# Performance work log

Measured on AMD Instinct MI355X. Metric: run time of the kernel, lower is better.

Reference implementation:

```python
import jax, jax.numpy as jnp
import numpy as np
from jax import lax

NC1, NC2, NC3 = 64, 64, 512
TEMP = 1.0
EPS = 1e-5
B = 256


def setup_inputs() -> dict:
    key = jax.random.key(0)
    ks = jax.random.split(key, 16)
    d = {}
    d["inp"] = jax.random.normal(ks[0], (B, 3, 32, 32), jnp.float32)
    d["conv1_w"] = jax.random.normal(ks[1], (6, 3, 5, 5), jnp.float32) * 0.1
    d["conv1_b"] = jax.random.normal(ks[2], (6,), jnp.float32) * 0.1
    d["bn1_g"] = jnp.ones((6,), jnp.float32)
    d["bn1_b"] = jnp.zeros((6,), jnp.float32)
    d["conv2_w"] = jax.random.normal(ks[3], (16, 6, 5, 5), jnp.float32) * 0.1
    d["conv2_b"] = jax.random.normal(ks[4], (16,), jnp.float32) * 0.1
    d["bn2_g"] = jnp.ones((16,), jnp.float32)
    d["bn2_b"] = jnp.zeros((16,), jnp.float32)
    d["fc1_w"] = jax.random.normal(ks[5], (120, 400), jnp.float32) * 0.05
    d["fc1_b"] = jax.random.normal(ks[6], (120,), jnp.float32) * 0.05
    d["fc2_w"] = jax.random.normal(ks[7], (10, 120), jnp.float32) * 0.05
    d["fc2_b"] = jax.random.normal(ks[8], (10,), jnp.float32) * 0.05
    d["k1s"] = jax.random.normal(ks[9], (NC1, 6), jnp.float32)
    d["k2s"] = jax.random.normal(ks[10], (NC2, 16), jnp.float32)
    d["k3s"] = jax.random.normal(ks[11], (NC3, 120), jnp.float32)
    return d


def _conv(x, w, b):
    y = lax.conv_general_dilated(x, w, (1, 1), 'VALID',
                                 dimension_numbers=('NCHW', 'OIHW', 'NCHW'))
    return y + b[None, :, None, None]


def _bn_train(x, g, b):
    # BatchNorm2d in training mode: biased batch stats over (N,H,W)
    mean = x.mean(axis=(0, 2, 3), keepdims=True)
    var = ((x - mean) ** 2).mean(axis=(0, 2, 3), keepdims=True)
    return (x - mean) / jnp.sqrt(var + EPS) * g[None, :, None, None] + b[None, :, None, None]


def _maxpool2(x):
    return lax.reduce_window(x, -jnp.inf, lax.max, (1, 1, 2, 2), (1, 1, 2, 2), 'VALID')


def _codebook_logits_spatial(act, keys):
    # act: [B,C,H,W], keys: [K,C] -> -||act - k||_2 over C -> [B,K,H,W]
    diff = act[:, None] - keys[None, :, :, None, None]
    return -jnp.sqrt((diff ** 2).sum(axis=2))


def _neural_gas_loss(v, temp):
    n_clusters = v.shape[1]
    weightings = jnp.exp(-jnp.arange(n_clusters, dtype=v.dtype) / temp)
    sorted_v = jnp.sort(v, axis=1)
    return (sorted_v ** 2 * weightings).sum(axis=1)


def reference(inp, conv1_w, conv1_b, bn1_g, bn1_b, conv2_w, conv2_b, bn2_g, bn2_b,
              fc1_w, fc1_b, fc2_w, fc2_b, k1s, k2s, k3s):
    act1 = _bn_train(_conv(inp, conv1_w, conv1_b), bn1_g, bn1_b)          # [B,6,28,28]
    act_logits1 = _codebook_logits_spatial(act1, k1s)                     # [B,NC1,28,28]
    x = _maxpool2(jax.nn.relu(act1))                                      # [B,6,14,14]
    act2 = _bn_train(_conv(x, conv2_w, conv2_b), bn2_g, bn2_b)            # [B,16,10,10]
    act_logits2 = _codebook_logits_spatial(act2, k2s)                     # [B,NC2,10,10]
    x = _maxpool2(jax.nn.relu(act2))                                      # [B,16,5,5]
    x = x.reshape(x.shape[0], -1)                                         # [B,400]
    act3 = x @ fc1_w.T + fc1_b                                            # [B,120]
    diff3 = act3[:, None, :] - k3s[None, :, :]
    act_logits3 = -jnp.sqrt((diff3 ** 2).sum(axis=2))                     # [B,NC3]
    x = jax.nn.relu(act3)
    act4 = x @ fc2_w.T + fc2_b                                            # [B,10]
    # ARGS.ng branch: neural-gas cluster loss + argmax assignments
    cluster_loss = _neural_gas_loss(act_logits3, TEMP)                    # [B]
    assignments = jnp.argmax(act_logits3, axis=1)                         # [B] int
    return (assignments, cluster_loss.mean(), act4, act_logits1, act_logits2, act_logits3)
```

## Files before the change

kernel.cpp:

```cpp
#include <hip/hip_runtime.h>

#define B 256
#define EPSV 1e-5f

#define OFF_ASSIGN 0
#define OFF_LOSS   256
#define OFF_ACT4   257
#define OFF_L1     2817
#define OFF_L2     12847873
#define OFF_L3     14486273

__device__ inline void wave_reduce2(float& s, float& q) {
#pragma unroll
    for (int o = 32; o > 0; o >>= 1) {
        s += __shfl_down(s, o, 64);
        q += __shfl_down(q, o, 64);
    }
}

__global__ __launch_bounds__(256) void conv1_kernel(
        const float* __restrict__ inp, const float* __restrict__ w,
        const float* __restrict__ bias, float* __restrict__ c1,
        float* __restrict__ part,
        const float* __restrict__ w1, const float* __restrict__ k3,
        float* __restrict__ w1t, float* __restrict__ k3st) {
    int bc = blockIdx.x;
    int tid = threadIdx.x;
    if (bc >= 1536) {
        int idx = (bc - 1536) * 256 + tid;
        if (idx < 48000) {
            int c = idx / 120, o = idx % 120;
            w1t[idx] = w1[o * 400 + c];
        } else if (idx < 48000 + 61440) {
            int j = idx - 48000;
            int c = j >> 9, k = j & 511;
            k3st[j] = k3[k * 120 + c];
        }
        return;
    }
    int b = bc / 6, c = bc % 6;
    __shared__ float ws[75];
    __shared__ float rs[4], rq[4];
    if (tid < 75) ws[tid] = w[c * 75 + tid];
    __syncthreads();
    const float* ip = inp + b * 3072;
    float bs = bias[c];
    float s = 0.f, sq = 0.f;
    for (int hw = tid; hw < 784; hw += 256) {
        int oh = hw / 28, ow = hw % 28;
        float acc = bs;
#pragma unroll
        for (int ic = 0; ic < 3; ++ic) {
            const float* ipc = ip + ic * 1024 + oh * 32 + ow;
            const float* wc = ws + ic * 25;
#pragma unroll
            for (int kh = 0; kh < 5; ++kh)
#pragma unroll
                for (int kw = 0; kw < 5; ++kw)
                    acc += ipc[kh * 32 + kw] * wc[kh * 5 + kw];
        }
        c1[bc * 784 + hw] = acc;
        s += acc; sq += acc * acc;
    }
    wave_reduce2(s, sq);
    if ((tid & 63) == 0) { rs[tid >> 6] = s; rq[tid >> 6] = sq; }
    __syncthreads();
    if (tid == 0) {
        part[bc * 2]     = rs[0] + rs[1] + rs[2] + rs[3];
        part[bc * 2 + 1] = rq[0] + rq[1] + rq[2] + rq[3];
    }
}

__global__ __launch_bounds__(1024) void stage1_kernel(
        const float* __restrict__ c1raw, const float* __restrict__ part1,
        const float* __restrict__ g1, const float* __restrict__ bb1,
        const float* __restrict__ k1s,
        const float* __restrict__ c2w, const float* __restrict__ c2b,
        float* __restrict__ outL1, float* __restrict__ c2,
        float* __restrict__ part2) {
    int b = blockIdx.x, tid = threadIdx.x;
    int lane = tid & 63, wid = tid >> 6;
    __shared__ float act[4704];
    __shared__ float sk[384];
    __shared__ float w2s[2400];
    __shared__ float xp[1176];
    __shared__ float sa[1600];
    __shared__ float chs[6], chq[6], ssc[6], ssh[6];
    if (wid < 6) {
        float s = 0.f, q = 0.f;
#pragma unroll
        for (int j = 0; j < 4; ++j) {
            int bi = lane + 64 * j;
            s += part1[(bi * 6 + wid) * 2];
            q += part1[(bi * 6 + wid) * 2 + 1];
        }
        wave_reduce2(s, q);
        if (lane == 0) { chs[wid] = s; chq[wid] = q; }
    }
    for (int i = tid; i < 384; i += 1024) sk[i] = k1s[i];
    for (int i = tid; i < 2400; i += 1024) w2s[i] = c2w[i];
    __syncthreads();
    if (tid < 6) {
        float m = chs[tid] * (1.f / 200704.f);
        float v = chq[tid] * (1.f / 200704.f) - m * m;
        float sc = g1[tid] * rsqrtf(v + EPSV);
        ssc[tid] = sc; ssh[tid] = bb1[tid] - m * sc;
    }
    __syncthreads();
    const float* cp = c1raw + b * 4704;
    for (int i = tid; i < 4704; i += 1024) {
        int c = i / 784;
        act[i] = cp[i] * ssc[c] + ssh[c];
    }
    __syncthreads();
    float* op = outL1 + (long)b * 50176;
    for (int i = tid; i < 50176; i += 1024) {
        int k = i / 784, hw = i - k * 784;
        const float* kp = sk + k * 6;
        float d0 = act[hw] - kp[0];
        float d1 = act[784 + hw] - kp[1];
        float d2 = act[1568 + hw] - kp[2];
        float d3 = act[2352 + hw] - kp[3];
        float d4 = act[3136 + hw] - kp[4];
        float d5 = act[3920 + hw] - kp[5];
        float s = d0 * d0 + d1 * d1 + d2 * d2 + d3 * d3 + d4 * d4 + d5 * d5;
        op[i] = -sqrtf(s);
    }
    for (int i = tid; i < 1176; i += 1024) {
        int c = i / 196, p = i % 196, ph = p / 14, pw = p % 14;
        const float* ap = act + c * 784 + ph * 56 + pw * 2;
        float m = fmaxf(fmaxf(ap[0], ap[1]), fmaxf(ap[28], ap[29]));
        xp[i] = fmaxf(m, 0.f);
    }
    __syncthreads();
    for (int i = tid; i < 1600; i += 1024) {
        int c = i / 100, hw = i - c * 100;
        int oh = hw / 10, ow = hw - oh * 10;
        float acc = c2b[c];
#pragma unroll
        for (int ic = 0; ic < 6; ++ic) {
            const float* xsrc = xp + ic * 196 + oh * 14 + ow;
            const float* wp = w2s + c * 150 + ic * 25;
#pragma unroll
            for (int kh = 0; kh < 5; ++kh)
#pragma unroll
                for (int kw = 0; kw < 5; ++kw)
                    acc += xsrc[kh * 14 + kw] * wp[kh * 5 + kw];
        }
        sa[i] = acc;
    }
    __syncthreads();
    for (int i = tid; i < 1600; i += 1024) c2[b * 1600 + i] = sa[i];
    {
        float s = 0.f, q = 0.f;
        if (lane < 100) { float x = sa[wid * 100 + lane]; s = x; q = x * x; }
        if (lane < 36)  { float x = sa[wid * 100 + 64 + lane]; s += x; q += x * x; }
        wave_reduce2(s, q);
        if (lane == 0) {
            part2[(b * 16 + wid) * 2]     = s;
            part2[(b * 16 + wid) * 2 + 1] = q;
        }
    }
}

__global__ __launch_bounds__(1024) void stage2_kernel(
        const float* __restrict__ c2, const float* __restrict__ part2,
        const float* __restrict__ g2, const float* __restrict__ bb2,
        const float* __restrict__ k2s,
        const float* __restrict__ w1t, const float* __restrict__ f1b,
        const float* __restrict__ f2w, const float* __restrict__ f2b,
        const float* __restrict__ k3st,
        float* __restrict__ outL2, float* __restrict__ outAct4,
        float* __restrict__ outL3, float* __restrict__ outAssign,
        float* __restrict__ lossb) {
    int b = blockIdx.x, tid = threadIdx.x;
    int lane = tid & 63, wid = tid >> 6;
    __shared__ float sa[1600];
    __shared__ float sk[1024];
    __shared__ float xs[400];
    __shared__ float chs[16], chq[16], ssc[16], ssh[16];
    __shared__ float partq[8][128];
    __shared__ float a3r[120], a3p[120];
    __shared__ float pv[2][512];
    __shared__ float sv[512];
    __shared__ int   cntp[2][512];
    __shared__ float wsum[8], wmv[8];
    __shared__ int wmi[8];
    {
        float s = 0.f, q = 0.f;
#pragma unroll
        for (int j = 0; j < 4; ++j) {
            int bi = lane + 64 * j;
            s += part2[(bi * 16 + wid) * 2];
            q += part2[(bi * 16 + wid) * 2 + 1];
        }
        wave_reduce2(s, q);
        if (lane == 0) { chs[wid] = s; chq[wid] = q; }
    }
    for (int i = tid; i < 1024; i += 1024) sk[i] = k2s[i];
    __syncthreads();
    if (tid < 16) {
        float m = chs[tid] * (1.f / 25600.f);
        float v = chq[tid] * (1.f / 25600.f) - m * m;
        float sc = g2[tid] * rsqrtf(v + EPSV);
        ssc[tid] = sc; ssh[tid] = bb2[tid] - m * sc;
    }
    __syncthreads();
    for (int i = tid; i < 1600; i += 1024) {
        int c = i / 100;
        sa[i] = c2[b * 1600 + i] * ssc[c] + ssh[c];
    }
    __syncthreads();
    float* op2 = outL2 + (long)b * 6400;
    for (int i = tid; i < 6400; i += 1024) {
        int k = i / 100, hw = i - k * 100;
        float s = 0.f;
#pragma unroll
        for (int c = 0; c < 16; ++c) {
            float d = sa[c * 100 + hw] - sk[k * 16 + c];
            s += d * d;
        }
        op2[i] = -sqrtf(s);
    }
    for (int i = tid; i < 400; i += 1024) {
        int c = i / 25, p = i % 25, ph = p / 5, pw = p % 5;
        const float* ap = sa + c * 100 + ph * 20 + pw * 2;
        float m = fmaxf(fmaxf(ap[0], ap[1]), fmaxf(ap[10], ap[11]));
        xs[i] = fmaxf(m, 0.f);
    }
    __syncthreads();
    {
        int o = tid & 127, q8 = tid >> 7;
        float s = 0.f;
        if (o < 120) {
            const float* wp = w1t + (q8 * 50) * 120 + o;
            const float* xp2 = xs + q8 * 50;
#pragma unroll 10
            for (int c = 0; c < 50; ++c) s += xp2[c] * wp[c * 120];
        }
        partq[q8][o] = s;
    }
    __syncthreads();
    if (tid < 120) {
        float acc = f1b[tid];
#pragma unroll
        for (int q8 = 0; q8 < 8; ++q8) acc += partq[q8][tid];
        a3r[tid] = acc;
        a3p[tid] = fmaxf(acc, 0.f);
    }
    __syncthreads();
    {
        int k = tid & 511, h = tid >> 9;
        const float* kp = k3st + k;
        float s = 0.f;
#pragma unroll 10
        for (int c = 0; c < 60; ++c) {
            int cc = h * 60 + c;
            float d = a3r[cc] - kp[cc * 512];
            s += d * d;
        }
        pv[h][k] = s;
    }
    if (tid < 10) {
        float acc = f2b[tid];
        const float* wp = f2w + tid * 120;
#pragma unroll 8
        for (int c = 0; c < 120; ++c) acc += a3p[c] * wp[c];
        outAct4[b * 10 + tid] = acc;
    }
    __syncthreads();
    if (tid < 512) {
        float v = -sqrtf(pv[0][tid] + pv[1][tid]);
        sv[tid] = v;
        outL3[(long)b * 512 + tid] = v;
    }
    __syncthreads();
    {
        int i = tid & 511, h = tid >> 9;
        float v = sv[i];
        const float4* sv4 = reinterpret_cast<const float4*>(sv);
        int cnt = 0;
#pragma unroll 8
        for (int j4 = h * 64; j4 < h * 64 + 64; ++j4) {
            float4 o4 = sv4[j4];
            int jb = j4 * 4;
            cnt += (o4.x < v || (o4.x == v && jb < i)) ? 1 : 0;
            cnt += (o4.y < v || (o4.y == v && jb + 1 < i)) ? 1 : 0;
            cnt += (o4.z < v || (o4.z == v && jb + 2 < i)) ? 1 : 0;
            cnt += (o4.w < v || (o4.w == v && jb + 3 < i)) ? 1 : 0;
        }
        cntp[h][i] = cnt;
    }
    __syncthreads();
    if (tid < 512) {
        float v = sv[tid];
        int cnt = cntp[0][tid] + cntp[1][tid];
        float contrib = v * v * expf(-(float)cnt);
        float ssum = contrib;
#pragma unroll
        for (int o = 32; o > 0; o >>= 1) ssum += __shfl_down(ssum, o, 64);
        float mv = v; int mi = tid;
#pragma unroll
        for (int o = 32; o > 0; o >>= 1) {
            float ov = __shfl_down(mv, o, 64);
            int oi = __shfl_down(mi, o, 64);
            if (ov > mv || (ov == mv && oi < mi)) { mv = ov; mi = oi; }
        }
        if (lane == 0) { wsum[wid] = ssum; wmv[wid] = mv; wmi[wid] = mi; }
    }
    __syncthreads();
    if (tid == 0) {
        float tot = 0.f;
        float bmv = wmv[0]; int bmi = wmi[0];
#pragma unroll
        for (int w = 0; w < 8; ++w) {
            tot += wsum[w];
            if (wmv[w] > bmv || (wmv[w] == bmv && wmi[w] < bmi)) { bmv = wmv[w]; bmi = wmi[w]; }
        }
        lossb[b] = tot;
        outAssign[b] = (float)bmi;
    }
}

__global__ void final_kernel(const float* __restrict__ loss_b, float* __restrict__ out_loss) {
    __shared__ float r[256];
    int tid = threadIdx.x;
    r[tid] = loss_b[tid];
    __syncthreads();
    for (int s = 128; s > 0; s >>= 1) {
        if (tid < s) r[tid] += r[tid + s];
        __syncthreads();
    }
    if (tid == 0) out_loss[0] = r[0] / 256.f;
}

extern "C" void kernel_launch(void* const* d_in, const int* in_sizes, int n_in,
                              void* d_out, int out_size, void* d_ws, size_t ws_size,
                              hipStream_t stream) {
    const float* inp = (const float*)d_in[0];
    const float* c1w = (const float*)d_in[1];
    const float* c1b = (const float*)d_in[2];
    const float* g1  = (const float*)d_in[3];
    const float* bb1 = (const float*)d_in[4];
    const float* c2w = (const float*)d_in[5];
    const float* c2b = (const float*)d_in[6];
    const float* g2  = (const float*)d_in[7];
    const float* bb2 = (const float*)d_in[8];
    const float* f1w = (const float*)d_in[9];
    const float* f1b = (const float*)d_in[10];
    const float* f2w = (const float*)d_in[11];
    const float* f2b = (const float*)d_in[12];
    const float* k1  = (const float*)d_in[13];
    const float* k2  = (const float*)d_in[14];
    const float* k3  = (const float*)d_in[15];
    float* out = (float*)d_out;

    float* W = (float*)d_ws;
    float* c1raw = W;
    float* part1 = c1raw + 1204224;
    float* c2raw = part1 + 3072;
    float* part2 = c2raw + 409600;
    float* lossb = part2 + 8192;
    float* w1t   = lossb + 256;
    float* k3st  = w1t + 48000;

    conv1_kernel<<<1964, 256, 0, stream>>>(inp, c1w, c1b, c1raw, part1,
                                           f1w, k3, w1t, k3st);
    stage1_kernel<<<B, 1024, 0, stream>>>(c1raw, part1, g1, bb1, k1, c2w, c2b,
                                          out + OFF_L1, c2raw, part2);
    stage2_kernel<<<B, 1024, 0, stream>>>(c2raw, part2, g2, bb2, k2,
                                          w1t, f1b, f2w, f2b, k3st,
                                          out + OFF_L2, out + OFF_ACT4,
                                          out + OFF_L3, out + OFF_ASSIGN, lossb);
    final_kernel<<<1, 256, 0, stream>>>(lossb, out + OFF_LOSS);
}
```

Before: 94.49 us.

## Fuse all stages into one persistent kernel with software grid barriers

Replaces the four kernel launches with a single 256-block kernel that keeps each sample's conv1 and conv2 activations in shared memory. Device-wide atomic barriers stand in for the launch boundaries needed by the batch-norm statistics, and the final loss reduction is done by block 0 after an atomic counter wait. This removes launch gaps and the global round trips of the conv1 and conv2 intermediates. In exchange, all 256 blocks must be co-resident for the spin barriers to be safe, block size drops from 1024 to 512, and a memset is added to reset the barrier counters.

```diff
diff --git a/kernel.cpp b/kernel.cpp
--- a/kernel.cpp
+++ b/kernel.cpp
@@ -10,7 +10,7 @@
 #define OFF_L2     12847873
 #define OFF_L3     14486273
 
-__device__ inline void wave_reduce2(float& s, float& q) {
+__device__ __forceinline__ void wave_reduce2(float& s, float& q) {
 #pragma unroll
     for (int o = 32; o > 0; o >>= 1) {
         s += __shfl_down(s, o, 64);
@@ -18,74 +18,110 @@
     }
 }
 
-__global__ __launch_bounds__(256) void conv1_kernel(
-        const float* __restrict__ inp, const float* __restrict__ w,
-        const float* __restrict__ bias, float* __restrict__ c1,
-        float* __restrict__ part,
-        const float* __restrict__ w1, const float* __restrict__ k3,
-        float* __restrict__ w1t, float* __restrict__ k3st) {
-    int bc = blockIdx.x;
-    int tid = threadIdx.x;
-    if (bc >= 1536) {
-        int idx = (bc - 1536) * 256 + tid;
-        if (idx < 48000) {
-            int c = idx / 120, o = idx % 120;
-            w1t[idx] = w1[o * 400 + c];
-        } else if (idx < 48000 + 61440) {
-            int j = idx - 48000;
-            int c = j >> 9, k = j & 511;
-            k3st[j] = k3[k * 120 + c];
-        }
-        return;
-    }
-    int b = bc / 6, c = bc % 6;
-    __shared__ float ws[75];
-    __shared__ float rs[4], rq[4];
-    if (tid < 75) ws[tid] = w[c * 75 + tid];
-    __syncthreads();
-    const float* ip = inp + b * 3072;
-    float bs = bias[c];
-    float s = 0.f, sq = 0.f;
-    for (int hw = tid; hw < 784; hw += 256) {
-        int oh = hw / 28, ow = hw % 28;
-        float acc = bs;
-#pragma unroll
-        for (int ic = 0; ic < 3; ++ic) {
-            const float* ipc = ip + ic * 1024 + oh * 32 + ow;
-            const float* wc = ws + ic * 25;
-#pragma unroll
-            for (int kh = 0; kh < 5; ++kh)
-#pragma unroll
-                for (int kw = 0; kw < 5; ++kw)
-                    acc += ipc[kh * 32 + kw] * wc[kh * 5 + kw];
-        }
-        c1[bc * 784 + hw] = acc;
-        s += acc; sq += acc * acc;
-    }
-    wave_reduce2(s, sq);
-    if ((tid & 63) == 0) { rs[tid >> 6] = s; rq[tid >> 6] = sq; }
-    __syncthreads();
-    if (tid == 0) {
-        part[bc * 2]     = rs[0] + rs[1] + rs[2] + rs[3];
-        part[bc * 2 + 1] = rq[0] + rq[1] + rq[2] + rq[3];
-    }
+__device__ __forceinline__ void gbar(unsigned* cnt, unsigned* gen) {
+    __syncthreads();
+    if (threadIdx.x == 0) {
+        __threadfence();
+        unsigned g = __hip_atomic_load(gen, __ATOMIC_RELAXED, __HIP_MEMORY_SCOPE_AGENT);
+        unsigned a = __hip_atomic_fetch_add(cnt, 1u, __ATOMIC_ACQ_REL, __HIP_MEMORY_SCOPE_AGENT);
+        if (a == gridDim.x - 1) {
+            __hip_atomic_store(cnt, 0u, __ATOMIC_RELAXED, __HIP_MEMORY_SCOPE_AGENT);
+            __hip_atomic_fetch_add(gen, 1u, __ATOMIC_RELEASE, __HIP_MEMORY_SCOPE_AGENT);
+        } else {
+            while (__hip_atomic_load(gen, __ATOMIC_ACQUIRE, __HIP_MEMORY_SCOPE_AGENT) == g)
+                __builtin_amdgcn_s_sleep(1);
+        }
+    }
+    __syncthreads();
 }
 
-__global__ __launch_bounds__(1024) void stage1_kernel(
-        const float* __restrict__ c1raw, const float* __restrict__ part1,
-        const float* __restrict__ g1, const float* __restrict__ bb1,
-        const float* __restrict__ k1s,
-        const float* __restrict__ c2w, const float* __restrict__ c2b,
-        float* __restrict__ outL1, float* __restrict__ c2,
-        float* __restrict__ part2) {
+__global__ __launch_bounds__(512, 4) void fused_kernel(
+        const float* __restrict__ inp, const float* __restrict__ c1w,
+        const float* __restrict__ c1b, const float* __restrict__ g1,
+        const float* __restrict__ bb1, const float* __restrict__ c2w,
+        const float* __restrict__ c2b, const float* __restrict__ g2,
+        const float* __restrict__ bb2, const float* __restrict__ f1w,
+        const float* __restrict__ f1b, const float* __restrict__ f2w,
+        const float* __restrict__ f2b, const float* __restrict__ k1s,
+        const float* __restrict__ k2s, const float* __restrict__ k3s,
+        float* __restrict__ out, unsigned* __restrict__ bar,
+        float* __restrict__ part1, float* __restrict__ part2,
+        float* __restrict__ lossb, float* __restrict__ w1t,
+        float* __restrict__ k3st) {
     int b = blockIdx.x, tid = threadIdx.x;
     int lane = tid & 63, wid = tid >> 6;
-    __shared__ float act[4704];
-    __shared__ float sk[384];
+
+    __shared__ __align__(16) float si[3072];
+    __shared__ __align__(16) float act[4704];
+    __shared__ float cw[450];
+    __shared__ float cb1[6];
+    __shared__ float sk1[384];
     __shared__ float w2s[2400];
+    __shared__ float c2bs[16];
     __shared__ float xp[1176];
     __shared__ float sa[1600];
-    __shared__ float chs[6], chq[6], ssc[6], ssh[6];
+    __shared__ float wpart[96];
+    __shared__ float chs[16], chq[16], ssc[16], ssh[16];
+    __shared__ float a3r[120], a3p[120];
+    __shared__ float wsum[8], wmv[8];
+    __shared__ int wmi[8];
+    __shared__ float rfin[256];
+    float* sk2   = si;
+    float* xs    = si + 1024;
+    float* partq = si + 1424;
+    float* sv    = si + 1936;
+
+    for (int i = tid; i < 3072; i += 512) si[i] = inp[b * 3072 + i];
+    for (int i = tid; i < 450; i += 512) cw[i] = c1w[i];
+    if (tid < 6) cb1[tid] = c1b[tid];
+    if (tid < 16) c2bs[tid] = c2b[tid];
+    for (int i = tid; i < 384; i += 512) sk1[i] = k1s[i];
+    for (int i = tid; i < 2400; i += 512) w2s[i] = c2w[i];
+    {
+        int idx = b * 428 + tid;
+        if (tid < 428 && idx < 109440) {
+            if (idx < 48000) { int c = idx / 120, o = idx % 120; w1t[idx] = f1w[o * 400 + c]; }
+            else { int j = idx - 48000; int c = j >> 9, k = j & 511; k3st[j] = k3s[k * 120 + c]; }
+        }
+    }
+    __syncthreads();
+    float s6[6], q6[6];
+#pragma unroll
+    for (int c = 0; c < 6; ++c) { s6[c] = 0.f; q6[c] = 0.f; }
+#pragma unroll
+    for (int c = 0; c < 6; ++c) {
+        for (int hw = tid; hw < 784; hw += 512) {
+            int oh = hw / 28, ow = hw % 28;
+            float acc = cb1[c];
+#pragma unroll
+            for (int ic = 0; ic < 3; ++ic) {
+                const float* ip = si + ic * 1024 + oh * 32 + ow;
+                const float* wp = cw + c * 75 + ic * 25;
+#pragma unroll
+                for (int kh = 0; kh < 5; ++kh)
+#pragma unroll
+                    for (int kw = 0; kw < 5; ++kw)
+                        acc += ip[kh * 32 + kw] * wp[kh * 5 + kw];
+            }
+            act[c * 784 + hw] = acc;
+            s6[c] += acc; q6[c] += acc * acc;
+        }
+    }
+#pragma unroll
+    for (int c = 0; c < 6; ++c) {
+        wave_reduce2(s6[c], q6[c]);
+        if (lane == 0) { wpart[(wid * 6 + c) * 2] = s6[c]; wpart[(wid * 6 + c) * 2 + 1] = q6[c]; }
+    }
+    __syncthreads();
+    if (tid < 6) {
+        float S = 0.f, Q = 0.f;
+#pragma unroll
+        for (int w = 0; w < 8; ++w) { S += wpart[(w * 6 + tid) * 2]; Q += wpart[(w * 6 + tid) * 2 + 1]; }
+        part1[(b * 6 + tid) * 2] = S;
+        part1[(b * 6 + tid) * 2 + 1] = Q;
+    }
+    gbar(bar + 0, bar + 1);
+
     if (wid < 6) {
         float s = 0.f, q = 0.f;
 #pragma unroll
@@ -97,8 +133,6 @@
         wave_reduce2(s, q);
         if (lane == 0) { chs[wid] = s; chq[wid] = q; }
     }
-    for (int i = tid; i < 384; i += 1024) sk[i] = k1s[i];
-    for (int i = tid; i < 2400; i += 1024) w2s[i] = c2w[i];
     __syncthreads();
     if (tid < 6) {
         float m = chs[tid] * (1.f / 200704.f);
@@ -107,36 +141,34 @@
         ssc[tid] = sc; ssh[tid] = bb1[tid] - m * sc;
     }
     __syncthreads();
-    const float* cp = c1raw + b * 4704;
-    for (int i = tid; i < 4704; i += 1024) {
+    for (int i = tid; i < 4704; i += 512) {
         int c = i / 784;
-        act[i] = cp[i] * ssc[c] + ssh[c];
-    }
-    __syncthreads();
-    float* op = outL1 + (long)b * 50176;
-    for (int i = tid; i < 50176; i += 1024) {
+        act[i] = act[i] * ssc[c] + ssh[c];
+    }
+    __syncthreads();
+    float* op = out + OFF_L1 + (long)b * 50176;
+    for (int i = tid; i < 50176; i += 512) {
         int k = i / 784, hw = i - k * 784;
-        const float* kp = sk + k * 6;
-        float d0 = act[hw] - kp[0];
-        float d1 = act[784 + hw] - kp[1];
+        const float* kp = sk1 + k * 6;
+        float d0 = act[hw]        - kp[0];
+        float d1 = act[784 + hw]  - kp[1];
         float d2 = act[1568 + hw] - kp[2];
         float d3 = act[2352 + hw] - kp[3];
         float d4 = act[3136 + hw] - kp[4];
         float d5 = act[3920 + hw] - kp[5];
-        float s = d0 * d0 + d1 * d1 + d2 * d2 + d3 * d3 + d4 * d4 + d5 * d5;
-        op[i] = -sqrtf(s);
-    }
-    for (int i = tid; i < 1176; i += 1024) {
+        op[i] = -sqrtf(d0*d0 + d1*d1 + d2*d2 + d3*d3 + d4*d4 + d5*d5);
+    }
+    for (int i = tid; i < 1176; i += 512) {
         int c = i / 196, p = i % 196, ph = p / 14, pw = p % 14;
         const float* ap = act + c * 784 + ph * 56 + pw * 2;
         float m = fmaxf(fmaxf(ap[0], ap[1]), fmaxf(ap[28], ap[29]));
         xp[i] = fmaxf(m, 0.f);
     }
     __syncthreads();
-    for (int i = tid; i < 1600; i += 1024) {
+    for (int i = tid; i < 1600; i += 512) {
         int c = i / 100, hw = i - c * 100;
         int oh = hw / 10, ow = hw - oh * 10;
-        float acc = c2b[c];
+        float acc = c2bs[c];
 #pragma unroll
         for (int ic = 0; ic < 6; ++ic) {
             const float* xsrc = xp + ic * 196 + oh * 14 + ow;
@@ -150,54 +182,31 @@
         sa[i] = acc;
     }
     __syncthreads();
-    for (int i = tid; i < 1600; i += 1024) c2[b * 1600 + i] = sa[i];
-    {
+#pragma unroll
+    for (int r = 0; r < 2; ++r) {
+        int cc = wid * 2 + r;
         float s = 0.f, q = 0.f;
-        if (lane < 100) { float x = sa[wid * 100 + lane]; s = x; q = x * x; }
-        if (lane < 36)  { float x = sa[wid * 100 + 64 + lane]; s += x; q += x * x; }
+        if (lane < 100) { float x = sa[cc * 100 + lane]; s = x; q = x * x; }
+        if (lane < 36)  { float x = sa[cc * 100 + 64 + lane]; s += x; q += x * x; }
         wave_reduce2(s, q);
-        if (lane == 0) {
-            part2[(b * 16 + wid) * 2]     = s;
-            part2[(b * 16 + wid) * 2 + 1] = q;
-        }
-    }
-}
-
-__global__ __launch_bounds__(1024) void stage2_kernel(
-        const float* __restrict__ c2, const float* __restrict__ part2,
-        const float* __restrict__ g2, const float* __restrict__ bb2,
-        const float* __restrict__ k2s,
-        const float* __restrict__ w1t, const float* __restrict__ f1b,
-        const float* __restrict__ f2w, const float* __restrict__ f2b,
-        const float* __restrict__ k3st,
-        float* __restrict__ outL2, float* __restrict__ outAct4,
-        float* __restrict__ outL3, float* __restrict__ outAssign,
-        float* __restrict__ lossb) {
-    int b = blockIdx.x, tid = threadIdx.x;
-    int lane = tid & 63, wid = tid >> 6;
-    __shared__ float sa[1600];
-    __shared__ float sk[1024];
-    __shared__ float xs[400];
-    __shared__ float chs[16], chq[16], ssc[16], ssh[16];
-    __shared__ float partq[8][128];
-    __shared__ float a3r[120], a3p[120];
-    __shared__ float pv[2][512];
-    __shared__ float sv[512];
-    __shared__ int   cntp[2][512];
-    __shared__ float wsum[8], wmv[8];
-    __shared__ int wmi[8];
-    {
+        if (lane == 0) { part2[(b * 16 + cc) * 2] = s; part2[(b * 16 + cc) * 2 + 1] = q; }
+    }
+    gbar(bar + 2, bar + 3);
+
+#pragma unroll
+    for (int r = 0; r < 2; ++r) {
+        int ch = wid + r * 8;
         float s = 0.f, q = 0.f;
 #pragma unroll
         for (int j = 0; j < 4; ++j) {
             int bi = lane + 64 * j;
-            s += part2[(bi * 16 + wid) * 2];
-            q += part2[(bi * 16 + wid) * 2 + 1];
+            s += part2[(bi * 16 + ch) * 2];
+            q += part2[(bi * 16 + ch) * 2 + 1];
         }
         wave_reduce2(s, q);
-        if (lane == 0) { chs[wid] = s; chq[wid] = q; }
-    }
-    for (int i = tid; i < 1024; i += 1024) sk[i] = k2s[i];
+        if (lane == 0) { chs[ch] = s; chq[ch] = q; }
+    }
+    for (int i = tid; i < 1024; i += 512) sk2[i] = k2s[i];
     __syncthreads();
     if (tid < 16) {
         float m = chs[tid] * (1.f / 25600.f);
@@ -206,23 +215,20 @@
         ssc[tid] = sc; ssh[tid] = bb2[tid] - m * sc;
     }
     __syncthreads();
-    for (int i = tid; i < 1600; i += 1024) {
+    for (int i = tid; i < 1600; i += 512) {
         int c = i / 100;
-        sa[i] = c2[b * 1600 + i] * ssc[c] + ssh[c];
-    }
-    __syncthreads();
-    float* op2 = outL2 + (long)b * 6400;
-    for (int i = tid; i < 6400; i += 1024) {
+        sa[i] = sa[i] * ssc[c] + ssh[c];
+    }
+    __syncthreads();
+    float* op2 = out + OFF_L2 + (long)b * 6400;
+    for (int i = tid; i < 6400; i += 512) {
         int k = i / 100, hw = i - k * 100;
         float s = 0.f;
 #pragma unroll
-        for (int c = 0; c < 16; ++c) {
-            float d = sa[c * 100 + hw] - sk[k * 16 + c];
-            s += d * d;
-        }
+        for (int c = 0; c < 16; ++c) { float d = sa[c * 100 + hw] - sk2[k * 16 + c]; s += d * d; }
         op2[i] = -sqrtf(s);
     }
-    for (int i = tid; i < 400; i += 1024) {
+    for (int i = tid; i < 400; i += 512) {
         int c = i / 25, p = i % 25, ph = p / 5, pw = p % 5;
         const float* ap = sa + c * 100 + ph * 20 + pw * 2;
         float m = fmaxf(fmaxf(ap[0], ap[1]), fmaxf(ap[10], ap[11]));
@@ -230,84 +236,64 @@
     }
     __syncthreads();
     {
-        int o = tid & 127, q8 = tid >> 7;
+        int o = tid & 127, q4 = tid >> 7;
         float s = 0.f;
         if (o < 120) {
-            const float* wp = w1t + (q8 * 50) * 120 + o;
-            const float* xp2 = xs + q8 * 50;
+            const float* wp = w1t + (q4 * 100) * 120 + o;
+            const float* xq = xs + q4 * 100;
 #pragma unroll 10
-            for (int c = 0; c < 50; ++c) s += xp2[c] * wp[c * 120];
-        }
-        partq[q8][o] = s;
+            for (int c = 0; c < 100; ++c) s += xq[c] * wp[c * 120];
+        }
+        partq[q4 * 128 + o] = s;
     }
     __syncthreads();
     if (tid < 120) {
-        float acc = f1b[tid];
-#pragma unroll
-        for (int q8 = 0; q8 < 8; ++q8) acc += partq[q8][tid];
+        float acc = f1b[tid] + partq[tid] + partq[128 + tid] + partq[256 + tid] + partq[384 + tid];
         a3r[tid] = acc;
         a3p[tid] = fmaxf(acc, 0.f);
     }
     __syncthreads();
+    float v;
     {
-        int k = tid & 511, h = tid >> 9;
-        const float* kp = k3st + k;
+        const float* kp = k3st + tid;
         float s = 0.f;
-#pragma unroll 10
-        for (int c = 0; c < 60; ++c) {
-            int cc = h * 60 + c;
-            float d = a3r[cc] - kp[cc * 512];
-            s += d * d;
-        }
-        pv[h][k] = s;
+#pragma unroll 8
+        for (int c = 0; c < 120; ++c) { float d = a3r[c] - kp[c * 512]; s += d * d; }
+        v = -sqrtf(s);
+        sv[tid] = v;
+        out[OFF_L3 + (long)b * 512 + tid] = v;
     }
     if (tid < 10) {
         float acc = f2b[tid];
         const float* wp = f2w + tid * 120;
 #pragma unroll 8
         for (int c = 0; c < 120; ++c) acc += a3p[c] * wp[c];
-        outAct4[b * 10 + tid] = acc;
-    }
-    __syncthreads();
-    if (tid < 512) {
-        float v = -sqrtf(pv[0][tid] + pv[1][tid]);
-        sv[tid] = v;
-        outL3[(long)b * 512 + tid] = v;
-    }
-    __syncthreads();
-    {
-        int i = tid & 511, h = tid >> 9;
-        float v = sv[i];
-        const float4* sv4 = reinterpret_cast<const float4*>(sv);
-        int cnt = 0;
+        out[OFF_ACT4 + b * 10 + tid] = acc;
+    }
+    __syncthreads();
+    const float4* sv4 = reinterpret_cast<const float4*>(sv);
+    int cnt = 0;
 #pragma unroll 8
-        for (int j4 = h * 64; j4 < h * 64 + 64; ++j4) {
-            float4 o4 = sv4[j4];
-            int jb = j4 * 4;
-            cnt += (o4.x < v || (o4.x == v && jb < i)) ? 1 : 0;
-            cnt += (o4.y < v || (o4.y == v && jb + 1 < i)) ? 1 : 0;
-            cnt += (o4.z < v || (o4.z == v && jb + 2 < i)) ? 1 : 0;
-            cnt += (o4.w < v || (o4.w == v && jb + 3 < i)) ? 1 : 0;
-        }
-        cntp[h][i] = cnt;
-    }
-    __syncthreads();
-    if (tid < 512) {
-        float v = sv[tid];
-        int cnt = cntp[0][tid] + cntp[1][tid];
-        float contrib = v * v * expf(-(float)cnt);
-        float ssum = contrib;
-#pragma unroll
-        for (int o = 32; o > 0; o >>= 1) ssum += __shfl_down(ssum, o, 64);
-        float mv = v; int mi = tid;
-#pragma unroll
-        for (int o = 32; o > 0; o >>= 1) {
-            float ov = __shfl_down(mv, o, 64);
-            int oi = __shfl_down(mi, o, 64);
-            if (ov > mv || (ov == mv && oi < mi)) { mv = ov; mi = oi; }
-        }
-        if (lane == 0) { wsum[wid] = ssum; wmv[wid] = mv; wmi[wid] = mi; }
-    }
+    for (int j4 = 0; j4 < 128; ++j4) {
+        float4 o4 = sv4[j4];
+        int jb = j4 * 4;
+        cnt += (o4.x < v || (o4.x == v && jb < tid)) ? 1 : 0;
+        cnt += (o4.y < v || (o4.y == v && jb + 1 < tid)) ? 1 : 0;
+        cnt += (o4.z < v || (o4.z == v && jb + 2 < tid)) ? 1 : 0;
+        cnt += (o4.w < v || (o4.w == v && jb + 3 < tid)) ? 1 : 0;
+    }
+    float contrib = v * v * expf(-(float)cnt);
+    float ssum = contrib;
+#pragma unroll
+    for (int o = 32; o > 0; o >>= 1) ssum += __shfl_down(ssum, o, 64);
+    float mv = v; int mi = tid;
+#pragma unroll
+    for (int o = 32; o > 0; o >>= 1) {
+        float ov = __shfl_down(mv, o, 64);
+        int oi = __shfl_down(mi, o, 64);
+        if (ov > mv || (ov == mv && oi < mi)) { mv = ov; mi = oi; }
+    }
+    if (lane == 0) { wsum[wid] = ssum; wmv[wid] = mv; wmi[wid] = mi; }
     __syncthreads();
     if (tid == 0) {
         float tot = 0.f;
@@ -318,20 +304,27 @@
             if (wmv[w] > bmv || (wmv[w] == bmv && wmi[w] < bmi)) { bmv = wmv[w]; bmi = wmi[w]; }
         }
         lossb[b] = tot;
-        outAssign[b] = (float)bmi;
-    }
-}
-
-__global__ void final_kernel(const float* __restrict__ loss_b, float* __restrict__ out_loss) {
-    __shared__ float r[256];
-    int tid = threadIdx.x;
-    r[tid] = loss_b[tid];
-    __syncthreads();
-    for (int s = 128; s > 0; s >>= 1) {
-        if (tid < s) r[tid] += r[tid + s];
+        out[OFF_ASSIGN + b] = (float)bmi;
+    }
+    __syncthreads();
+
+    if (tid == 0) {
+        __threadfence();
+        __hip_atomic_fetch_add(bar + 4, 1u, __ATOMIC_ACQ_REL, __HIP_MEMORY_SCOPE_AGENT);
+    }
+    if (b != 0) return;
+    if (tid == 0) {
+        while (__hip_atomic_load(bar + 4, __ATOMIC_ACQUIRE, __HIP_MEMORY_SCOPE_AGENT) < 256u)
+            __builtin_amdgcn_s_sleep(1);
+    }
+    __syncthreads();
+    if (tid < 256) rfin[tid] = lossb[tid];
+    __syncthreads();
+    for (int s2 = 128; s2 > 0; s2 >>= 1) {
+        if (tid < s2 && tid < 256) rfin[tid] += rfin[tid + s2];
         __syncthreads();
     }
-    if (tid == 0) out_loss[0] = r[0] / 256.f;
+    if (tid == 0) out[OFF_LOSS] = rfin[0] * (1.f / 256.f);
 }
 
 extern "C" void kernel_launch(void* const* d_in, const int* in_sizes, int n_in,
@@ -356,21 +349,15 @@
     float* out = (float*)d_out;
 
     float* W = (float*)d_ws;
-    float* c1raw = W;
-    float* part1 = c1raw + 1204224;
-    float* c2raw = part1 + 3072;
-    float* part2 = c2raw + 409600;
-    float* lossb = part2 + 8192;
-    float* w1t   = lossb + 256;
-    float* k3st  = w1t + 48000;
-
-    conv1_kernel<<<1964, 256, 0, stream>>>(inp, c1w, c1b, c1raw, part1,
-                                           f1w, k3, w1t, k3st);
-    stage1_kernel<<<B, 1024, 0, stream>>>(c1raw, part1, g1, bb1, k1, c2w, c2b,
-                                          out + OFF_L1, c2raw, part2);
-    stage2_kernel<<<B, 1024, 0, stream>>>(c2raw, part2, g2, bb2, k2,
-                                          w1t, f1b, f2w, f2b, k3st,
-                                          out + OFF_L2, out + OFF_ACT4,
-                                          out + OFF_L3, out + OFF_ASSIGN, lossb);
-    final_kernel<<<1, 256, 0, stream>>>(lossb, out + OFF_LOSS);
+    unsigned* bar = (unsigned*)d_ws;
+    float* part1 = W + 64;
+    float* part2 = W + 3136;
+    float* lossb = W + 11328;
+    float* w1t   = W + 11584;
+    float* k3st  = W + 59584;
+
+    hipMemsetAsync(d_ws, 0, 64, stream);
+    fused_kernel<<<B, 512, 0, stream>>>(inp, c1w, c1b, g1, bb1, c2w, c2b, g2, bb2,
+                                        f1w, f1b, f2w, f2b, k1, k2, k3,
+                                        out, bar, part1, part2, lossb, w1t, k3st);
 }
```

After: 151.3 us. 1.6x slower.

## Split per-sample stage kernels across more blocks and use dot-product distance expansion

Applied to the files above, without the earlier changes.

Stage1 now launches four 512-thread blocks per sample, and each block writes a quarter of the 64 codebook-1 distance maps. Only the first block of each sample goes on to compute conv2. Stage2 uses three blocks per sample: two compute halves of the codebook-2 distances and one handles the FC layers, codebook-3 and the ranking. Distances are computed as ||a||^2 + ||k||^2 - 2·a·k, which cuts per-element work but adds cancellation risk, clamped at zero. The split also spreads work across more CUs, at the cost of re-normalizing the activations redundantly in every block.

```diff
diff --git a/kernel.cpp b/kernel.cpp
--- a/kernel.cpp
+++ b/kernel.cpp
@@ -10,7 +10,7 @@
 #define OFF_L2     12847873
 #define OFF_L3     14486273
 
-__device__ inline void wave_reduce2(float& s, float& q) {
+__device__ __forceinline__ void wave_reduce2(float& s, float& q) {
 #pragma unroll
     for (int o = 32; o > 0; o >>= 1) {
         s += __shfl_down(s, o, 64);
@@ -71,21 +71,24 @@
     }
 }
 
-__global__ __launch_bounds__(1024) void stage1_kernel(
+__global__ __launch_bounds__(512) void stage1_kernel(
         const float* __restrict__ c1raw, const float* __restrict__ part1,
         const float* __restrict__ g1, const float* __restrict__ bb1,
         const float* __restrict__ k1s,
         const float* __restrict__ c2w, const float* __restrict__ c2b,
-        float* __restrict__ outL1, float* __restrict__ c2,
+        float* __restrict__ out, float* __restrict__ c2raw,
         float* __restrict__ part2) {
-    int b = blockIdx.x, tid = threadIdx.x;
+    int b = blockIdx.x >> 2, h = blockIdx.x & 3;
+    int tid = threadIdx.x;
     int lane = tid & 63, wid = tid >> 6;
-    __shared__ float act[4704];
-    __shared__ float sk[384];
+    __shared__ __align__(16) float act[4704];
+    __shared__ float sk1[384], k2sq1[64];
+    __shared__ float chs[6], chq[6], ssc[6], ssh[6];
+    __shared__ float xp[1176];
     __shared__ float w2s[2400];
-    __shared__ float xp[1176];
-    __shared__ float sa[1600];
-    __shared__ float chs[6], chq[6], ssc[6], ssh[6];
+    if (tid < 384) sk1[tid] = k1s[tid];
+    if (h == 0) for (int i = tid; i < 2400; i += 512) w2s[i] = c2w[i];
+    __syncthreads();
     if (wid < 6) {
         float s = 0.f, q = 0.f;
 #pragma unroll
@@ -97,8 +100,13 @@
         wave_reduce2(s, q);
         if (lane == 0) { chs[wid] = s; chq[wid] = q; }
     }
-    for (int i = tid; i < 384; i += 1024) sk[i] = k1s[i];
-    for (int i = tid; i < 2400; i += 1024) w2s[i] = c2w[i];
+    if (tid >= 384 && tid < 448) {
+        int k = tid - 384;
+        float s = 0.f;
+#pragma unroll
+        for (int c = 0; c < 6; ++c) { float x = sk1[k * 6 + c]; s += x * x; }
+        k2sq1[k] = s;
+    }
     __syncthreads();
     if (tid < 6) {
         float m = chs[tid] * (1.f / 200704.f);
@@ -107,33 +115,35 @@
         ssc[tid] = sc; ssh[tid] = bb1[tid] - m * sc;
     }
     __syncthreads();
-    const float* cp = c1raw + b * 4704;
-    for (int i = tid; i < 4704; i += 1024) {
+    for (int i = tid; i < 4704; i += 512) {
         int c = i / 784;
-        act[i] = cp[i] * ssc[c] + ssh[c];
-    }
-    __syncthreads();
-    float* op = outL1 + (long)b * 50176;
-    for (int i = tid; i < 50176; i += 1024) {
-        int k = i / 784, hw = i - k * 784;
-        const float* kp = sk + k * 6;
-        float d0 = act[hw] - kp[0];
-        float d1 = act[784 + hw] - kp[1];
-        float d2 = act[1568 + hw] - kp[2];
-        float d3 = act[2352 + hw] - kp[3];
-        float d4 = act[3136 + hw] - kp[4];
-        float d5 = act[3920 + hw] - kp[5];
-        float s = d0 * d0 + d1 * d1 + d2 * d2 + d3 * d3 + d4 * d4 + d5 * d5;
-        op[i] = -sqrtf(s);
-    }
-    for (int i = tid; i < 1176; i += 1024) {
+        act[i] = c1raw[b * 4704 + i] * ssc[c] + ssh[c];
+    }
+    __syncthreads();
+    for (int hw = tid; hw < 784; hw += 512) {
+        float a0 = act[hw], a1 = act[784 + hw], a2 = act[1568 + hw];
+        float a3 = act[2352 + hw], a4 = act[3136 + hw], a5 = act[3920 + hw];
+        float A2 = a0*a0 + a1*a1 + a2*a2 + a3*a3 + a4*a4 + a5*a5;
+        float* op = out + OFF_L1 + (long)b * 50176 + (h * 16) * 784 + hw;
+#pragma unroll
+        for (int kk = 0; kk < 16; ++kk) {
+            int k = h * 16 + kk;
+            const float* kp = sk1 + k * 6;
+            float dot = a0*kp[0] + a1*kp[1] + a2*kp[2] + a3*kp[3] + a4*kp[4] + a5*kp[5];
+            op[kk * 784] = -sqrtf(fmaxf(A2 + k2sq1[k] - 2.f * dot, 0.f));
+        }
+    }
+    if (h != 0) return;
+    __syncthreads();
+    for (int i = tid; i < 1176; i += 512) {
         int c = i / 196, p = i % 196, ph = p / 14, pw = p % 14;
         const float* ap = act + c * 784 + ph * 56 + pw * 2;
         float m = fmaxf(fmaxf(ap[0], ap[1]), fmaxf(ap[28], ap[29]));
         xp[i] = fmaxf(m, 0.f);
     }
     __syncthreads();
-    for (int i = tid; i < 1600; i += 1024) {
+    float* sa = act;
+    for (int i = tid; i < 1600; i += 512) {
         int c = i / 100, hw = i - c * 100;
         int oh = hw / 10, ow = hw - oh * 10;
         float acc = c2b[c];
@@ -148,56 +158,58 @@
                     acc += xsrc[kh * 14 + kw] * wp[kh * 5 + kw];
         }
         sa[i] = acc;
-    }
-    __syncthreads();
-    for (int i = tid; i < 1600; i += 1024) c2[b * 1600 + i] = sa[i];
-    {
+        c2raw[b * 1600 + i] = acc;
+    }
+    __syncthreads();
+#pragma unroll
+    for (int r = 0; r < 2; ++r) {
+        int cc = wid * 2 + r;
         float s = 0.f, q = 0.f;
-        if (lane < 100) { float x = sa[wid * 100 + lane]; s = x; q = x * x; }
-        if (lane < 36)  { float x = sa[wid * 100 + 64 + lane]; s += x; q += x * x; }
+        if (lane < 100) { float x = sa[cc * 100 + lane]; s = x; q = x * x; }
+        if (lane < 36)  { float x = sa[cc * 100 + 64 + lane]; s += x; q += x * x; }
         wave_reduce2(s, q);
-        if (lane == 0) {
-            part2[(b * 16 + wid) * 2]     = s;
-            part2[(b * 16 + wid) * 2 + 1] = q;
-        }
-    }
-}
-
-__global__ __launch_bounds__(1024) void stage2_kernel(
-        const float* __restrict__ c2, const float* __restrict__ part2,
+        if (lane == 0) { part2[(b * 16 + cc) * 2] = s; part2[(b * 16 + cc) * 2 + 1] = q; }
+    }
+}
+
+__global__ __launch_bounds__(512) void stage2_kernel(
+        const float* __restrict__ c2raw, const float* __restrict__ part2,
         const float* __restrict__ g2, const float* __restrict__ bb2,
         const float* __restrict__ k2s,
         const float* __restrict__ w1t, const float* __restrict__ f1b,
         const float* __restrict__ f2w, const float* __restrict__ f2b,
         const float* __restrict__ k3st,
-        float* __restrict__ outL2, float* __restrict__ outAct4,
-        float* __restrict__ outL3, float* __restrict__ outAssign,
-        float* __restrict__ lossb) {
-    int b = blockIdx.x, tid = threadIdx.x;
+        float* __restrict__ out, float* __restrict__ lossb) {
+    int bh = blockIdx.x;
+    int b = bh / 3, h = bh - b * 3;
+    int tid = threadIdx.x;
     int lane = tid & 63, wid = tid >> 6;
-    __shared__ float sa[1600];
-    __shared__ float sk[1024];
+    __shared__ __align__(16) float sa[1600];
+    __shared__ float sk2[1024], k2sq2[64], A2s[112];
+    __shared__ float chs[16], chq[16], ssc[16], ssh[16];
     __shared__ float xs[400];
-    __shared__ float chs[16], chq[16], ssc[16], ssh[16];
-    __shared__ float partq[8][128];
+    __shared__ float partq[512];
     __shared__ float a3r[120], a3p[120];
-    __shared__ float pv[2][512];
-    __shared__ float sv[512];
-    __shared__ int   cntp[2][512];
+    __shared__ __align__(16) float sv[512];
     __shared__ float wsum[8], wmv[8];
     __shared__ int wmi[8];
+    sk2[tid] = k2s[tid];
+    sk2[tid + 512] = k2s[tid + 512];
     {
-        float s = 0.f, q = 0.f;
-#pragma unroll
-        for (int j = 0; j < 4; ++j) {
-            int bi = lane + 64 * j;
-            s += part2[(bi * 16 + wid) * 2];
-            q += part2[(bi * 16 + wid) * 2 + 1];
-        }
-        wave_reduce2(s, q);
-        if (lane == 0) { chs[wid] = s; chq[wid] = q; }
-    }
-    for (int i = tid; i < 1024; i += 1024) sk[i] = k2s[i];
+#pragma unroll
+        for (int r = 0; r < 2; ++r) {
+            int ch = wid + r * 8;
+            float s = 0.f, q = 0.f;
+#pragma unroll
+            for (int j = 0; j < 4; ++j) {
+                int bi = lane + 64 * j;
+                s += part2[(bi * 16 + ch) * 2];
+                q += part2[(bi * 16 + ch) * 2 + 1];
+            }
+            wave_reduce2(s, q);
+            if (lane == 0) { chs[ch] = s; chq[ch] = q; }
+        }
+    }
     __syncthreads();
     if (tid < 16) {
         float m = chs[tid] * (1.f / 25600.f);
@@ -205,24 +217,41 @@
         float sc = g2[tid] * rsqrtf(v + EPSV);
         ssc[tid] = sc; ssh[tid] = bb2[tid] - m * sc;
     }
-    __syncthreads();
-    for (int i = tid; i < 1600; i += 1024) {
+    if (tid >= 64 && tid < 128) {
+        int k = tid - 64;
+        float s = 0.f;
+#pragma unroll
+        for (int c = 0; c < 16; ++c) { float x = sk2[k * 16 + c]; s += x * x; }
+        k2sq2[k] = s;
+    }
+    __syncthreads();
+    for (int i = tid; i < 1600; i += 512) {
         int c = i / 100;
-        sa[i] = c2[b * 1600 + i] * ssc[c] + ssh[c];
-    }
-    __syncthreads();
-    float* op2 = outL2 + (long)b * 6400;
-    for (int i = tid; i < 6400; i += 1024) {
-        int k = i / 100, hw = i - k * 100;
-        float s = 0.f;
-#pragma unroll
-        for (int c = 0; c < 16; ++c) {
-            float d = sa[c * 100 + hw] - sk[k * 16 + c];
-            s += d * d;
-        }
-        op2[i] = -sqrtf(s);
-    }
-    for (int i = tid; i < 400; i += 1024) {
+        sa[i] = c2raw[b * 1600 + i] * ssc[c] + ssh[c];
+    }
+    __syncthreads();
+    if (tid < 100) {
+        float s = 0.f;
+#pragma unroll
+        for (int c = 0; c < 16; ++c) { float a = sa[c * 100 + tid]; s += a * a; }
+        A2s[tid] = s;
+    }
+    __syncthreads();
+    if (h != 0) {
+        int kb = (h - 1) * 32;
+        for (int i = tid; i < 3200; i += 512) {
+            int kk = i / 100, hw = i - kk * 100;
+            int k = kb + kk;
+            const float* kp = sk2 + k * 16;
+            float dot = 0.f;
+#pragma unroll
+            for (int c = 0; c < 16; ++c) dot += sa[c * 100 + hw] * kp[c];
+            out[OFF_L2 + (long)b * 6400 + k * 100 + hw] =
+                -sqrtf(fmaxf(A2s[hw] + k2sq2[k] - 2.f * dot, 0.f));
+        }
+        return;
+    }
+    for (int i = tid; i < 400; i += 512) {
         int c = i / 25, p = i % 25, ph = p / 5, pw = p % 5;
         const float* ap = sa + c * 100 + ph * 20 + pw * 2;
         float m = fmaxf(fmaxf(ap[0], ap[1]), fmaxf(ap[10], ap[11]));
@@ -230,84 +259,64 @@
     }
     __syncthreads();
     {
-        int o = tid & 127, q8 = tid >> 7;
+        int o = tid & 127, q4 = tid >> 7;
         float s = 0.f;
         if (o < 120) {
-            const float* wp = w1t + (q8 * 50) * 120 + o;
-            const float* xp2 = xs + q8 * 50;
+            const float* wp = w1t + (q4 * 100) * 120 + o;
+            const float* xq = xs + q4 * 100;
 #pragma unroll 10
-            for (int c = 0; c < 50; ++c) s += xp2[c] * wp[c * 120];
-        }
-        partq[q8][o] = s;
+            for (int c = 0; c < 100; ++c) s += xq[c] * wp[c * 120];
+        }
+        partq[q4 * 128 + o] = s;
     }
     __syncthreads();
     if (tid < 120) {
-        float acc = f1b[tid];
-#pragma unroll
-        for (int q8 = 0; q8 < 8; ++q8) acc += partq[q8][tid];
+        float acc = f1b[tid] + partq[tid] + partq[128 + tid] + partq[256 + tid] + partq[384 + tid];
         a3r[tid] = acc;
         a3p[tid] = fmaxf(acc, 0.f);
     }
     __syncthreads();
+    float v;
     {
-        int k = tid & 511, h = tid >> 9;
-        const float* kp = k3st + k;
-        float s = 0.f;
-#pragma unroll 10
-        for (int c = 0; c < 60; ++c) {
-            int cc = h * 60 + c;
-            float d = a3r[cc] - kp[cc * 512];
-            s += d * d;
-        }
-        pv[h][k] = s;
+        const float* kp = k3st + tid;
+        float s = 0.f;
+#pragma unroll 8
+        for (int c = 0; c < 120; ++c) { float d = a3r[c] - kp[c * 512]; s += d * d; }
+        v = -sqrtf(s);
+        sv[tid] = v;
+        out[OFF_L3 + (long)b * 512 + tid] = v;
     }
     if (tid < 10) {
         float acc = f2b[tid];
         const float* wp = f2w + tid * 120;
 #pragma unroll 8
         for (int c = 0; c < 120; ++c) acc += a3p[c] * wp[c];
-        outAct4[b * 10 + tid] = acc;
-    }
-    __syncthreads();
-    if (tid < 512) {
-        float v = -sqrtf(pv[0][tid] + pv[1][tid]);
-        sv[tid] = v;
-        outL3[(long)b * 512 + tid] = v;
-    }
-    __syncthreads();
-    {
-        int i = tid & 511, h = tid >> 9;
-        float v = sv[i];
-        const float4* sv4 = reinterpret_cast<const float4*>(sv);
-        int cnt = 0;
+        out[OFF_ACT4 + b * 10 + tid] = acc;
+    }
+    __syncthreads();
+    const float4* sv4 = reinterpret_cast<const float4*>(sv);
+    int cnt = 0;
 #pragma unroll 8
-        for (int j4 = h * 64; j4 < h * 64 + 64; ++j4) {
-            float4 o4 = sv4[j4];
-            int jb = j4 * 4;
-            cnt += (o4.x < v || (o4.x == v && jb < i)) ? 1 : 0;
-            cnt += (o4.y < v || (o4.y == v && jb + 1 < i)) ? 1 : 0;
-            cnt += (o4.z < v || (o4.z == v && jb + 2 < i)) ? 1 : 0;
-            cnt += (o4.w < v || (o4.w == v && jb + 3 < i)) ? 1 : 0;
-        }
-        cntp[h][i] = cnt;
-    }
-    __syncthreads();
-    if (tid < 512) {
-        float v = sv[tid];
-        int cnt = cntp[0][tid] + cntp[1][tid];
-        float contrib = v * v * expf(-(float)cnt);
-        float ssum = contrib;
-#pragma unroll
-        for (int o = 32; o > 0; o >>= 1) ssum += __shfl_down(ssum, o, 64);
-        float mv = v; int mi = tid;
-#pragma unroll
-        for (int o = 32; o > 0; o >>= 1) {
-            float ov = __shfl_down(mv, o, 64);
-            int oi = __shfl_down(mi, o, 64);
-            if (ov > mv || (ov == mv && oi < mi)) { mv = ov; mi = oi; }
-        }
-        if (lane == 0) { wsum[wid] = ssum; wmv[wid] = mv; wmi[wid] = mi; }
-    }
+    for (int j4 = 0; j4 < 128; ++j4) {
+        float4 o4 = sv4[j4];
+        int jb = j4 * 4;
+        cnt += (o4.x < v || (o4.x == v && jb < tid)) ? 1 : 0;
+        cnt += (o4.y < v || (o4.y == v && jb + 1 < tid)) ? 1 : 0;
+        cnt += (o4.z < v || (o4.z == v && jb + 2 < tid)) ? 1 : 0;
+        cnt += (o4.w < v || (o4.w == v && jb + 3 < tid)) ? 1 : 0;
+    }
+    float contrib = v * v * expf(-(float)cnt);
+    float ssum = contrib;
+#pragma unroll
+    for (int o = 32; o > 0; o >>= 1) ssum += __shfl_down(ssum, o, 64);
+    float mv = v; int mi = tid;
+#pragma unroll
+    for (int o = 32; o > 0; o >>= 1) {
+        float ov = __shfl_down(mv, o, 64);
+        int oi = __shfl_down(mi, o, 64);
+        if (ov > mv || (ov == mv && oi < mi)) { mv = ov; mi = oi; }
+    }
+    if (lane == 0) { wsum[wid] = ssum; wmv[wid] = mv; wmi[wid] = mi; }
     __syncthreads();
     if (tid == 0) {
         float tot = 0.f;
@@ -318,7 +327,7 @@
             if (wmv[w] > bmv || (wmv[w] == bmv && wmi[w] < bmi)) { bmv = wmv[w]; bmi = wmi[w]; }
         }
         lossb[b] = tot;
-        outAssign[b] = (float)bmi;
+        out[OFF_ASSIGN + b] = (float)bmi;
     }
 }
 
@@ -366,11 +375,9 @@
 
     conv1_kernel<<<1964, 256, 0, stream>>>(inp, c1w, c1b, c1raw, part1,
                                            f1w, k3, w1t, k3st);
-    stage1_kernel<<<B, 1024, 0, stream>>>(c1raw, part1, g1, bb1, k1, c2w, c2b,
-                                          out + OFF_L1, c2raw, part2);
-    stage2_kernel<<<B, 1024, 0, stream>>>(c2raw, part2, g2, bb2, k2,
-                                          w1t, f1b, f2w, f2b, k3st,
-                                          out + OFF_L2, out + OFF_ACT4,
-                                          out + OFF_L3, out + OFF_ASSIGN, lossb);
+    stage1_kernel<<<B * 4, 512, 0, stream>>>(c1raw, part1, g1, bb1, k1, c2w, c2b,
+                                             out, c2raw, part2);
+    stage2_kernel<<<B * 3, 512, 0, stream>>>(c2raw, part2, g2, bb2, k2,
+                                             w1t, f1b, f2w, f2b, k3st, out, lossb);
     final_kernel<<<1, 256, 0, stream>>>(lossb, out + OFF_LOSS);
 }
```

After: 144.6 us. 53.1% more time.
